# Optimization experiments

Measured on AMD Instinct MI355X. Metric: run time of the kernel, lower is better.

The kernel has to match this reference:

```python
import jax, jax.numpy as jnp
import numpy as np

V = 20000   # token vocab (num_embeddings)
SC = 4000   # sub-char vocab (new_size of sub_char embedding)
D = 128     # embedding_dim
L = 15      # max nodes per decomposition tree (<= 8 leaves)
B, S = 32, 512


def _build_trees(rng):
    """Random binary decomposition trees in topological order (children < parent)."""
    node_ids = np.zeros((V, L), np.int32)
    left = np.full((V, L), -1, np.int32)
    right = np.full((V, L), -1, np.int32)
    last = np.zeros((V,), np.int32)
    for v in range(V):
        n_leaves = int(rng.integers(2, 9))
        stack, nodes = [], []
        leaves_left = n_leaves
        while leaves_left > 0 or len(stack) > 1:
            if leaves_left > 0 and (len(stack) < 2 or rng.random() < 0.5):
                nodes.append((-1, -1)); leaves_left -= 1
            else:
                r = stack.pop(); l = stack.pop()
                nodes.append((l, r))
            stack.append(len(nodes) - 1)
        n = len(nodes)
        for j, (l, r) in enumerate(nodes):
            left[v, j] = l; right[v, j] = r
        node_ids[v, :n] = rng.integers(0, SC, n)
        last[v] = n - 1
    return node_ids, left, right, last


def setup_inputs() -> dict:
    key = jax.random.key(0)
    k1, k2, k3, k4 = jax.random.split(key, 4)
    rng = np.random.default_rng(0)
    node_ids, left, right, last = _build_trees(rng)
    inp = {
        "input": jax.random.randint(k1, (B, S), 0, V, dtype=jnp.int32),
        "node_ids": jnp.asarray(node_ids),
        "left": jnp.asarray(left),
        "right": jnp.asarray(right),
        "last": jnp.asarray(last),
        "emb": jax.random.normal(k2, (SC, 5 * D), jnp.float32) * 0.1,   # sub_char weights
        "Wlh_w": jax.random.normal(k3, (D, 5 * D), jnp.float32) * 0.05,  # Linear(D,5D), x @ W
        "Wlh_b": jnp.zeros((5 * D,), jnp.float32),
        "Wrh_w": jax.random.normal(k4, (D, 5 * D), jnp.float32) * 0.05,
        "Wrh_b": jnp.zeros((5 * D,), jnp.float32),
    }
    return inp


def _tree_lstm(node_ids, left, right, last, emb, Wlh_w, Wlh_b, Wrh_w, Wrh_b):
    nV, nL = node_ids.shape
    gv = jnp.arange(nV)

    def step(carry, xs):
        h_all, c_all = carry                  # [V, L, D] each
        ids, l, r, j = xs                     # [V], [V], [V], scalar
        is_int = (l >= 0)[:, None]            # internal node mask; leaf has l==r==-1
        li, ri = jnp.maximum(l, 0), jnp.maximum(r, 0)
        hl, hr = h_all[gv, li], h_all[gv, ri]  # gather children states [V, D]
        cl, cr = c_all[gv, li], c_all[gv, ri]
        s = emb[ids]                           # [V, 5D]
        s_int = s + (hl @ Wlh_w + Wlh_b) + (hr @ Wrh_w + Wrh_b)
        s = jnp.where(is_int, s_int, s)
        ig, lfg, rfg, og, ug = jnp.split(s, 5, axis=1)
        c = jax.nn.sigmoid(ig) * jnp.tanh(ug)
        c = c + jnp.where(is_int, jax.nn.sigmoid(lfg) * cl + jax.nn.sigmoid(rfg) * cr, 0.0)
        h = jax.nn.sigmoid(og) * jnp.tanh(c)
        h_all = h_all.at[:, j].set(h)
        c_all = c_all.at[:, j].set(c)
        return (h_all, c_all), None

    init = (jnp.zeros((nV, nL, emb.shape[1] // 5), emb.dtype),
            jnp.zeros((nV, nL, emb.shape[1] // 5), emb.dtype))
    xs = (node_ids.T, left.T, right.T, jnp.arange(nL))
    (h_all, _), _ = jax.lax.scan(step, init, xs)
    return h_all[gv, last]                     # root h per vocab entry [V, D]


def reference(input, node_ids, left, right, last, emb, Wlh_w, Wlh_b, Wrh_w, Wrh_b):
    lut = _tree_lstm(node_ids, left, right, last, emb, Wlh_w, Wlh_b, Wrh_w, Wrh_b)  # [V, D]
    return lut[input]                          # [B, S, D]
```

## Files before the change

### kernel.cpp

```cpp
#include <hip/hip_runtime.h>
#include <hip/hip_fp16.h>
#include <math.h>

#define V    20000
#define SCV  4000
#define LL   15
#define OUTN (16384 * 128)

#define LEAF_BIT 0x40000000
#define REF_MASK 0x3FFFFFFF
#define ROOT_BIT 0x20000000
#define SLOT_MASK 0x1FFFFFFF
#define DUMMY_SLOT 89999

#define OFF_COUNTS 0
#define OFF_ROOT   128
#define OFF_LISTS  80384
#define OFF_LEAFC  5968384
#define OFF_LEAFHH 8016384
#define OFF_WT     19280384
#define OFF_BIAS   19608064
#define OFF_HINT   19610624
#define OFF_CINT   65690624
#define OFF_HH     111770624
#define OFF_USED   134810624

__device__ __constant__ int d_listOff[8] = {0, 0, 80000, 120000, 160000, 180000, 200000, 220000};

#define MT 128

typedef _Float16 f16x8 __attribute__((ext_vector_type(8)));
typedef float    f32x4 __attribute__((ext_vector_type(4)));

__device__ __forceinline__ float sigm(float x) { return 1.0f / (1.0f + expf(-x)); }

__global__ void prep_kernel(const int* __restrict__ input,
                            const float* __restrict__ emb,
                            const float* __restrict__ Wl, const float* __restrict__ Wlb,
                            const float* __restrict__ Wr, const float* __restrict__ Wrb,
                            float* __restrict__ leafC, __half* __restrict__ leafHh,
                            __half* __restrict__ WT, float* __restrict__ biasSum,
                            unsigned char* __restrict__ used) {
    __shared__ float T[64][65];
    int t = threadIdx.x, bid = blockIdx.x;
    for (int r = bid * 2 + (t >> 7); r < SCV; r += gridDim.x * 2) {
        int i = t & 127;
        const float* e = emb + r * 640;
        float c = sigm(e[i]) * tanhf(e[512 + i]);
        float h = sigm(e[384 + i]) * tanhf(c);
        leafC[r * 128 + i] = c;
        leafHh[r * 128 + i] = __float2half(h);
    }
    for (int i = bid * 256 + t; i < 16384; i += gridDim.x * 256)
        used[input[i]] = 1;
    if (bid == 41)
        for (int i = t; i < 640; i += 256) biasSum[i] = Wlb[i] + Wrb[i];
    if (bid < 40) {
        int kb = (bid & 3) * 64, nb = (bid >> 2) * 64;
        int tx = t & 63, ty = t >> 6;
        for (int kk = ty; kk < 64; kk += 4) {
            int k = kb + kk;
            const float* Wsrc = (k < 128) ? (Wl + k * 640) : (Wr + (k - 128) * 640);
            T[kk][tx] = Wsrc[nb + tx];
        }
        __syncthreads();
        for (int nn = ty; nn < 64; nn += 4)
            WT[(nb + nn) * 256 + kb + tx] = __float2half(T[tx][nn]);
    }
}

__global__ void meta_kernel(const int* __restrict__ node_ids,
                            const int* __restrict__ left,
                            const int* __restrict__ right,
                            const int* __restrict__ last,
                            const unsigned char* __restrict__ used,
                            int* __restrict__ counts,
                            int* __restrict__ rootSlot,
                            int4* __restrict__ lists) {
    __shared__ int  sHei[MT][17];
    __shared__ int  sRef[MT][17];
    __shared__ int4 ebuf[MT][7];
    __shared__ int  ebin[MT][7];
    __shared__ int  locCnt[8];
    __shared__ int  basePos[8];
    __shared__ int  scanBuf[MT];
    __shared__ int  blockBase;

    int tid = threadIdx.x;
    if (tid < 8) locCnt[tid] = 0;
    __syncthreads();

    int v = blockIdx.x * MT + tid;
    int nInt = 0;
    if (v < V && used[v]) {
        int l15[LL], r15[LL], id15[LL];
#pragma unroll
        for (int j = 0; j < LL; ++j) {
            l15[j]  = left[v * LL + j];
            r15[j]  = right[v * LL + j];
            id15[j] = node_ids[v * LL + j];
        }
        int lastv = last[v];
#pragma unroll
        for (int j = 0; j < LL; ++j) {
            if (j <= lastv) {
                int l = l15[j];
                if (l < 0) {
                    sHei[tid][j] = 0;
                    sRef[tid][j] = LEAF_BIT | id15[j];
                } else {
                    int r = r15[j];
                    int hl = sHei[tid][l], hr = sHei[tid][r];
                    int hh = 1 + (hl > hr ? hl : hr);
                    sHei[tid][j] = hh;
                    int pos = atomicAdd(&locCnt[hh], 1);
                    int flag = (j == lastv) ? ROOT_BIT : 0;
                    ebuf[tid][nInt] = make_int4(nInt | flag, id15[j], sRef[tid][l], sRef[tid][r]);
                    ebin[tid][nInt] = (hh << 16) | pos;
                    sRef[tid][j] = nInt;
                    ++nInt;
                }
            }
        }
    }
    scanBuf[tid] = nInt;
    __syncthreads();
    for (int d = 1; d < MT; d <<= 1) {
        int val = (tid >= d) ? scanBuf[tid - d] : 0;
        __syncthreads();
        scanBuf[tid] += val;
        __syncthreads();
    }
    if (tid == 0) blockBase = atomicAdd(&counts[31], scanBuf[MT - 1]);
    if (tid < 8) {
        int c = locCnt[tid];
        basePos[tid] = c ? atomicAdd(&counts[tid], c) : 0;
    }
    __syncthreads();
    int treeBase = blockBase + scanBuf[tid] - nInt;
    if (v < V && nInt > 0) rootSlot[v] = treeBase + nInt - 1;
    for (int e = 0; e < nInt; ++e) {
        int4 E  = ebuf[tid][e];
        int md  = ebin[tid][e];
        int hh  = md >> 16, pos = md & 0xFFFF;
        E.x += treeBase;
        E.z = (E.z & LEAF_BIT) ? E.z : (E.z + treeBase);
        E.w = (E.w & LEAF_BIT) ? E.w : (E.w + treeBase);
        lists[d_listOff[hh] + basePos[hh] + pos] = E;
    }
}

__launch_bounds__(512, 4)
__global__ void round_mfma(const int4* __restrict__ list, const int* __restrict__ cntPtr,
                           const float* __restrict__ emb, const __half* __restrict__ WT,
                           const float* __restrict__ biasSum,
                           const __half* __restrict__ leafHh, const float* __restrict__ leafC,
                           float* __restrict__ hInt, float* __restrict__ cInt,
                           __half* __restrict__ hH) {
    __shared__ __half Ah[32][264];
    __shared__ int4 meta[32];
    int cnt = *cntPtr;
    int nGroups = (cnt + 31) >> 5;
    int t = threadIdx.x;
    int lane = t & 63, wave = t >> 6;
    int ln15 = lane & 15, quad = lane >> 4;
    for (int grp = blockIdx.x; grp < nGroups; grp += gridDim.x) {
        int base = grp * 32;
        int rows = cnt - base; if (rows > 32) rows = 32;
        if (t < 32) {
            int4 E;
            if (t < rows) E = list[base + t];
            else { E.x = DUMMY_SLOT; E.y = 0; E.z = LEAF_BIT; E.w = LEAF_BIT; }
            meta[t] = E;
        }
        __syncthreads();
#pragma unroll
        for (int it = 0; it < 2; ++it) {
            int idx = t + it * 512;
            int m = idx >> 5, q = idx & 31;
            int ref = (q < 16) ? meta[m].z : meta[m].w;
            const __half* hs = (ref & LEAF_BIT) ? leafHh : hH;
            uint4 v = *(const uint4*)(hs + (ref & REF_MASK) * 128 + (q & 15) * 8);
            *(uint4*)(&Ah[m][q * 8]) = v;
        }
        float bs[5];
#pragma unroll
        for (int p = 0; p < 5; ++p) bs[p] = biasSum[p * 128 + 16 * wave + ln15];
        f32x4 acc[2][5];
#pragma unroll
        for (int c = 0; c < 2; ++c)
#pragma unroll
            for (int r = 0; r < 4; ++r) {
                const float* eb = emb + meta[c * 16 + quad * 4 + r].y * 640 + 16 * wave + ln15;
#pragma unroll
                for (int p = 0; p < 5; ++p)
                    acc[c][p][r] = eb[p * 128] + bs[p];
            }
        __syncthreads();
        const __half* wbase = WT + (16 * wave + ln15) * 256 + quad * 8;
#pragma unroll 2
        for (int kb = 0; kb < 8; ++kb) {
            f16x8 bf[5];
#pragma unroll
            for (int p = 0; p < 5; ++p)
                bf[p] = *(const f16x8*)((const void*)(wbase + p * 32768 + kb * 32));
            f16x8 af[2];
#pragma unroll
            for (int c = 0; c < 2; ++c)
                af[c] = *(const f16x8*)((const void*)&Ah[c * 16 + ln15][kb * 32 + quad * 8]);
#pragma unroll
            for (int p = 0; p < 5; ++p)
#pragma unroll
                for (int c = 0; c < 2; ++c)
                    acc[c][p] = __builtin_amdgcn_mfma_f32_16x16x32_f16(af[c], bf[p], acc[c][p], 0, 0, 0);
        }
        int d = 16 * wave + ln15;
#pragma unroll
        for (int c = 0; c < 2; ++c)
#pragma unroll
            for (int r = 0; r < 4; ++r) {
                int4 E = meta[c * 16 + quad * 4 + r];
                float ig = acc[c][0][r], lfg = acc[c][1][r], rfg = acc[c][2][r];
                float og = acc[c][3][r], ug = acc[c][4][r];
                float cl = ((E.z & LEAF_BIT) ? leafC : cInt)[(E.z & REF_MASK) * 128 + d];
                float cr = ((E.w & LEAF_BIT) ? leafC : cInt)[(E.w & REF_MASK) * 128 + d];
                float cc = sigm(ig) * tanhf(ug) + sigm(lfg) * cl + sigm(rfg) * cr;
                float hh2 = sigm(og) * tanhf(cc);
                int slot = E.x & SLOT_MASK;
                if (E.x & ROOT_BIT) {
                    hInt[slot * 128 + d] = hh2;
                } else {
                    cInt[slot * 128 + d] = cc;
                    hH[slot * 128 + d] = __float2half(hh2);
                }
            }
        __syncthreads();
    }
}

__global__ void gather_kernel(const int* __restrict__ input,
                              const int* __restrict__ rootSlot,
                              const float* __restrict__ hInt,
                              float4* __restrict__ out) {
    int idx = blockIdx.x * 256 + threadIdx.x;
    int token = input[idx >> 5];
    int d = idx & 31;
    out[idx] = ((const float4*)hInt)[rootSlot[token] * 32 + d];
}

extern "C" void kernel_launch(void* const* d_in, const int* in_sizes, int n_in,
                              void* d_out, int out_size, void* d_ws, size_t ws_size,
                              hipStream_t stream) {
    const int*   input    = (const int*)d_in[0];
    const int*   node_ids = (const int*)d_in[1];
    const int*   left     = (const int*)d_in[2];
    const int*   right    = (const int*)d_in[3];
    const int*   last     = (const int*)d_in[4];
    const float* emb      = (const float*)d_in[5];
    const float* Wl       = (const float*)d_in[6];
    const float* Wlb      = (const float*)d_in[7];
    const float* Wr       = (const float*)d_in[8];
    const float* Wrb      = (const float*)d_in[9];
    float* out = (float*)d_out;

    char* ws = (char*)d_ws;
    int*    counts   = (int*)(ws + OFF_COUNTS);
    int*    rootSlot = (int*)(ws + OFF_ROOT);
    int4*   lists    = (int4*)(ws + OFF_LISTS);
    float*  leafC    = (float*)(ws + OFF_LEAFC);
    __half* leafHh   = (__half*)(ws + OFF_LEAFHH);
    __half* WT       = (__half*)(ws + OFF_WT);
    float*  biasSum  = (float*)(ws + OFF_BIAS);
    float*  hInt     = (float*)(ws + OFF_HINT);
    float*  cInt     = (float*)(ws + OFF_CINT);
    __half* hH       = (__half*)(ws + OFF_HH);
    unsigned char* usedp = (unsigned char*)(ws + OFF_USED);

    (void)hipMemsetAsync(counts, 0, 128, stream);
    (void)hipMemsetAsync(usedp, 0, V, stream);

    prep_kernel<<<1024, 256, 0, stream>>>(input, emb, Wl, Wlb, Wr, Wrb,
                                          leafC, leafHh, WT, biasSum, usedp);
    meta_kernel<<<(V + MT - 1) / MT, MT, 0, stream>>>(node_ids, left, right, last, usedp,
                                                      counts, rootSlot, lists);

    static const int h_listOff[8] = {0, 0, 80000, 120000, 160000, 180000, 200000, 220000};
    static const int h_grid[8]    = {0, 1024, 512, 256, 128, 32, 16, 8};
    for (int h = 1; h <= 7; ++h) {
        round_mfma<<<h_grid[h], 512, 0, stream>>>(
            lists + h_listOff[h], counts + h,
            emb, WT, biasSum, leafHh, leafC, hInt, cInt, hH);
    }

    gather_kernel<<<OUTN / 4 / 256, 256, 0, stream>>>(input, rootSlot, hInt, (float4*)out);
}
```

Before: 326.2 us.

## Load MFMA A-fragments directly from global memory and drop the shared-memory staging

The round kernel no longer stages child hidden states and metadata in shared memory. Each lane now loads its MFMA A-operand fragments straight from the global leaf/internal half tables and reads list entries directly, so all three __syncthreads per group go away. Bias and weight base pointers are hoisted out of the group loop, and the k-loop is fully unrolled. In exchange, every wave re-reads the same A rows and list entries from global/L2 instead of sharing one staged copy, which adds redundant memory traffic.

```diff
diff --git a/kernel.cpp b/kernel.cpp
--- a/kernel.cpp
+++ b/kernel.cpp
@@ -157,69 +157,66 @@
                            const __half* __restrict__ leafHh, const float* __restrict__ leafC,
                            float* __restrict__ hInt, float* __restrict__ cInt,
                            __half* __restrict__ hH) {
-    __shared__ __half Ah[32][264];
-    __shared__ int4 meta[32];
     int cnt = *cntPtr;
     int nGroups = (cnt + 31) >> 5;
     int t = threadIdx.x;
     int lane = t & 63, wave = t >> 6;
     int ln15 = lane & 15, quad = lane >> 4;
+    float bs[5];
+#pragma unroll
+    for (int p = 0; p < 5; ++p) bs[p] = biasSum[p * 128 + 16 * wave + ln15];
+    const __half* wbase = WT + (16 * wave + ln15) * 256 + quad * 8;
+    int d = 16 * wave + ln15;
+
     for (int grp = blockIdx.x; grp < nGroups; grp += gridDim.x) {
         int base = grp * 32;
-        int rows = cnt - base; if (rows > 32) rows = 32;
-        if (t < 32) {
-            int4 E;
-            if (t < rows) E = list[base + t];
-            else { E.x = DUMMY_SLOT; E.y = 0; E.z = LEAF_BIT; E.w = LEAF_BIT; }
-            meta[t] = E;
-        }
-        __syncthreads();
-#pragma unroll
-        for (int it = 0; it < 2; ++it) {
-            int idx = t + it * 512;
-            int m = idx >> 5, q = idx & 31;
-            int ref = (q < 16) ? meta[m].z : meta[m].w;
-            const __half* hs = (ref & LEAF_BIT) ? leafHh : hH;
-            uint4 v = *(const uint4*)(hs + (ref & REF_MASK) * 128 + (q & 15) * 8);
-            *(uint4*)(&Ah[m][q * 8]) = v;
-        }
-        float bs[5];
-#pragma unroll
-        for (int p = 0; p < 5; ++p) bs[p] = biasSum[p * 128 + 16 * wave + ln15];
+        const __half* aP[2][2];
+#pragma unroll
+        for (int c = 0; c < 2; ++c) {
+            int m = c * 16 + ln15;
+            int rz = LEAF_BIT, rw = LEAF_BIT;
+            if (base + m < cnt) { int4 E = list[base + m]; rz = E.z; rw = E.w; }
+            aP[c][0] = ((rz & LEAF_BIT) ? leafHh : hH) + (rz & REF_MASK) * 128;
+            aP[c][1] = ((rw & LEAF_BIT) ? leafHh : hH) + (rw & REF_MASK) * 128;
+        }
         f32x4 acc[2][5];
 #pragma unroll
         for (int c = 0; c < 2; ++c)
 #pragma unroll
             for (int r = 0; r < 4; ++r) {
-                const float* eb = emb + meta[c * 16 + quad * 4 + r].y * 640 + 16 * wave + ln15;
+                int m = c * 16 + quad * 4 + r;
+                int id = (base + m < cnt) ? list[base + m].y : 0;
+                const float* eb = emb + id * 640 + d;
 #pragma unroll
                 for (int p = 0; p < 5; ++p)
                     acc[c][p][r] = eb[p * 128] + bs[p];
             }
-        __syncthreads();
-        const __half* wbase = WT + (16 * wave + ln15) * 256 + quad * 8;
-#pragma unroll 2
+#pragma unroll
         for (int kb = 0; kb < 8; ++kb) {
+            const int side = kb >> 2;
+            const int ko   = (kb & 3) * 32 + quad * 8;
+            f16x8 af[2];
+#pragma unroll
+            for (int c = 0; c < 2; ++c)
+                af[c] = *(const f16x8*)((const void*)(aP[c][side] + ko));
             f16x8 bf[5];
 #pragma unroll
             for (int p = 0; p < 5; ++p)
                 bf[p] = *(const f16x8*)((const void*)(wbase + p * 32768 + kb * 32));
-            f16x8 af[2];
-#pragma unroll
-            for (int c = 0; c < 2; ++c)
-                af[c] = *(const f16x8*)((const void*)&Ah[c * 16 + ln15][kb * 32 + quad * 8]);
 #pragma unroll
             for (int p = 0; p < 5; ++p)
 #pragma unroll
                 for (int c = 0; c < 2; ++c)
                     acc[c][p] = __builtin_amdgcn_mfma_f32_16x16x32_f16(af[c], bf[p], acc[c][p], 0, 0, 0);
         }
-        int d = 16 * wave + ln15;
 #pragma unroll
         for (int c = 0; c < 2; ++c)
 #pragma unroll
             for (int r = 0; r < 4; ++r) {
-                int4 E = meta[c * 16 + quad * 4 + r];
+                int m = c * 16 + quad * 4 + r;
+                int4 E;
+                if (base + m < cnt) E = list[base + m];
+                else { E.x = DUMMY_SLOT; E.y = 0; E.z = LEAF_BIT; E.w = LEAF_BIT; }
                 float ig = acc[c][0][r], lfg = acc[c][1][r], rfg = acc[c][2][r];
                 float og = acc[c][3][r], ug = acc[c][4][r];
                 float cl = ((E.z & LEAF_BIT) ? leafC : cInt)[(E.z & REF_MASK) * 128 + d];
@@ -234,7 +231,6 @@
                     hH[slot * 128 + d] = __float2half(hh2);
                 }
             }
-        __syncthreads();
     }
 }
 
```

Result: slower. 522.2 us (+60.1%).

## Fuse last tree levels into one persistent kernel with grid barriers; fp16 packed embedding

Applied to the files above, without the earlier changes.

Merges the three smallest height rounds (5-7) into a single 8-block kernel that steps through the levels with a software grid barrier. This removes two kernel launches and their gaps. It also precomputes an fp16 gate-interleaved embedding table, so each row needs one 16-byte load instead of five strided fp32 loads, and it hoists the bias and weight-pointer setup out of the group loop. The risks are reduced embedding precision, extra prep work, and a spin barrier that relies on all 8 blocks being co-resident; the barrier counters sit in the counts area that is zeroed each call.

```diff
diff --git a/kernel.cpp b/kernel.cpp
--- a/kernel.cpp
+++ b/kernel.cpp
@@ -18,6 +18,7 @@
 #define OFF_LISTS  80384
 #define OFF_LEAFC  5968384
 #define OFF_LEAFHH 8016384
+#define OFF_EMBT   9040384
 #define OFF_WT     19280384
 #define OFF_BIAS   19608064
 #define OFF_HINT   19610624
@@ -39,6 +40,7 @@
                             const float* __restrict__ Wl, const float* __restrict__ Wlb,
                             const float* __restrict__ Wr, const float* __restrict__ Wrb,
                             float* __restrict__ leafC, __half* __restrict__ leafHh,
+                            __half* __restrict__ embT,
                             __half* __restrict__ WT, float* __restrict__ biasSum,
                             unsigned char* __restrict__ used) {
     __shared__ float T[64][65];
@@ -50,6 +52,15 @@
         float h = sigm(e[384 + i]) * tanhf(c);
         leafC[r * 128 + i] = c;
         leafHh[r * 128 + i] = __float2half(h);
+    }
+    for (int idx = bid * 256 + t; idx < SCV * 128; idx += gridDim.x * 256) {
+        int id = idx >> 7, dd = idx & 127;
+        const float* e = emb + id * 640 + dd;
+        __half v[8];
+#pragma unroll
+        for (int p = 0; p < 5; ++p) v[p] = __float2half(e[p * 128]);
+        v[5] = __float2half(0.f); v[6] = v[5]; v[7] = v[5];
+        *(uint4*)(embT + (size_t)idx * 8) = *(const uint4*)v;
     }
     for (int i = bid * 256 + t; i < 16384; i += gridDim.x * 256)
         used[input[i]] = 1;
@@ -150,20 +161,25 @@
     }
 }
 
-__launch_bounds__(512, 4)
-__global__ void round_mfma(const int4* __restrict__ list, const int* __restrict__ cntPtr,
-                           const float* __restrict__ emb, const __half* __restrict__ WT,
-                           const float* __restrict__ biasSum,
-                           const __half* __restrict__ leafHh, const float* __restrict__ leafC,
-                           float* __restrict__ hInt, float* __restrict__ cInt,
-                           __half* __restrict__ hH) {
-    __shared__ __half Ah[32][264];
-    __shared__ int4 meta[32];
-    int cnt = *cntPtr;
+__device__ __forceinline__ void round_body(const int4* __restrict__ list, int cnt,
+                                           const __half* __restrict__ embT,
+                                           const __half* __restrict__ WT,
+                                           const float* __restrict__ biasSum,
+                                           const __half* __restrict__ leafHh,
+                                           const float* __restrict__ leafC,
+                                           float* __restrict__ hInt, float* __restrict__ cInt,
+                                           __half* __restrict__ hH,
+                                           __half (*Ah)[264], int4* meta) {
     int nGroups = (cnt + 31) >> 5;
     int t = threadIdx.x;
     int lane = t & 63, wave = t >> 6;
     int ln15 = lane & 15, quad = lane >> 4;
+    int d = 16 * wave + ln15;
+    float bs[5];
+#pragma unroll
+    for (int p = 0; p < 5; ++p) bs[p] = biasSum[p * 128 + d];
+    const __half* wbase = WT + d * 256 + quad * 8;
+
     for (int grp = blockIdx.x; grp < nGroups; grp += gridDim.x) {
         int base = grp * 32;
         int rows = cnt - base; if (rows > 32) rows = 32;
@@ -183,21 +199,18 @@
             uint4 v = *(const uint4*)(hs + (ref & REF_MASK) * 128 + (q & 15) * 8);
             *(uint4*)(&Ah[m][q * 8]) = v;
         }
-        float bs[5];
-#pragma unroll
-        for (int p = 0; p < 5; ++p) bs[p] = biasSum[p * 128 + 16 * wave + ln15];
         f32x4 acc[2][5];
 #pragma unroll
         for (int c = 0; c < 2; ++c)
 #pragma unroll
             for (int r = 0; r < 4; ++r) {
-                const float* eb = emb + meta[c * 16 + quad * 4 + r].y * 640 + 16 * wave + ln15;
+                int id = meta[c * 16 + quad * 4 + r].y;
+                f16x8 ev = *(const f16x8*)((const void*)(embT + ((size_t)id * 128 + d) * 8));
 #pragma unroll
                 for (int p = 0; p < 5; ++p)
-                    acc[c][p][r] = eb[p * 128] + bs[p];
+                    acc[c][p][r] = (float)ev[p] + bs[p];
             }
         __syncthreads();
-        const __half* wbase = WT + (16 * wave + ln15) * 256 + quad * 8;
 #pragma unroll 2
         for (int kb = 0; kb < 8; ++kb) {
             f16x8 bf[5];
@@ -214,7 +227,6 @@
                 for (int c = 0; c < 2; ++c)
                     acc[c][p] = __builtin_amdgcn_mfma_f32_16x16x32_f16(af[c], bf[p], acc[c][p], 0, 0, 0);
         }
-        int d = 16 * wave + ln15;
 #pragma unroll
         for (int c = 0; c < 2; ++c)
 #pragma unroll
@@ -238,6 +250,48 @@
     }
 }
 
+__launch_bounds__(512, 4)
+__global__ void round_mfma(const int4* __restrict__ list, const int* __restrict__ cntPtr,
+                           const __half* __restrict__ embT, const __half* __restrict__ WT,
+                           const float* __restrict__ biasSum,
+                           const __half* __restrict__ leafHh, const float* __restrict__ leafC,
+                           float* __restrict__ hInt, float* __restrict__ cInt,
+                           __half* __restrict__ hH) {
+    __shared__ __half Ah[32][264];
+    __shared__ int4 meta[32];
+    round_body(list, *cntPtr, embT, WT, biasSum, leafHh, leafC, hInt, cInt, hH, Ah, meta);
+}
+
+__device__ __forceinline__ void grid_barrier_n(int* bar, int n) {
+    __syncthreads();
+    if (threadIdx.x == 0) {
+        __threadfence();
+        __hip_atomic_fetch_add(bar, 1, __ATOMIC_RELAXED, __HIP_MEMORY_SCOPE_AGENT);
+        while (__hip_atomic_load(bar, __ATOMIC_RELAXED, __HIP_MEMORY_SCOPE_AGENT) < n)
+            __builtin_amdgcn_s_sleep(8);
+        __threadfence();
+    }
+    __syncthreads();
+}
+
+#define NTAIL 8
+__launch_bounds__(512, 4)
+__global__ void tail_mfma(const int4* __restrict__ lists, const int* __restrict__ counts,
+                          const __half* __restrict__ embT, const __half* __restrict__ WT,
+                          const float* __restrict__ biasSum,
+                          const __half* __restrict__ leafHh, const float* __restrict__ leafC,
+                          float* __restrict__ hInt, float* __restrict__ cInt,
+                          __half* __restrict__ hH, int* __restrict__ bar) {
+    __shared__ __half Ah[32][264];
+    __shared__ int4 meta[32];
+#pragma unroll 1
+    for (int h = 5; h <= 7; ++h) {
+        round_body(lists + d_listOff[h], counts[h], embT, WT, biasSum,
+                   leafHh, leafC, hInt, cInt, hH, Ah, meta);
+        if (h < 7) grid_barrier_n(&bar[h - 5], NTAIL);
+    }
+}
+
 __global__ void gather_kernel(const int* __restrict__ input,
                               const int* __restrict__ rootSlot,
                               const float* __restrict__ hInt,
@@ -269,6 +323,7 @@
     int4*   lists    = (int4*)(ws + OFF_LISTS);
     float*  leafC    = (float*)(ws + OFF_LEAFC);
     __half* leafHh   = (__half*)(ws + OFF_LEAFHH);
+    __half* embT     = (__half*)(ws + OFF_EMBT);
     __half* WT       = (__half*)(ws + OFF_WT);
     float*  biasSum  = (float*)(ws + OFF_BIAS);
     float*  hInt     = (float*)(ws + OFF_HINT);
@@ -280,17 +335,19 @@
     (void)hipMemsetAsync(usedp, 0, V, stream);
 
     prep_kernel<<<1024, 256, 0, stream>>>(input, emb, Wl, Wlb, Wr, Wrb,
-                                          leafC, leafHh, WT, biasSum, usedp);
+                                          leafC, leafHh, embT, WT, biasSum, usedp);
     meta_kernel<<<(V + MT - 1) / MT, MT, 0, stream>>>(node_ids, left, right, last, usedp,
                                                       counts, rootSlot, lists);
 
     static const int h_listOff[8] = {0, 0, 80000, 120000, 160000, 180000, 200000, 220000};
-    static const int h_grid[8]    = {0, 1024, 512, 256, 128, 32, 16, 8};
-    for (int h = 1; h <= 7; ++h) {
+    static const int h_grid[8]    = {0, 1024, 512, 256, 128, 0, 0, 0};
+    for (int h = 1; h <= 4; ++h) {
         round_mfma<<<h_grid[h], 512, 0, stream>>>(
             lists + h_listOff[h], counts + h,
-            emb, WT, biasSum, leafHh, leafC, hInt, cInt, hH);
-    }
+            embT, WT, biasSum, leafHh, leafC, hInt, cInt, hH);
+    }
+    tail_mfma<<<NTAIL, 512, 0, stream>>>(lists, counts, embT, WT, biasSum,
+                                         leafHh, leafC, hInt, cInt, hH, counts + 16);
 
     gather_kernel<<<OUTN / 4 / 256, 256, 0, stream>>>(input, rootSlot, hInt, (float4*)out);
 }
```

Result: slower. 467.6 us (+43.4%).
